# Optimization experiments

Hardware: AMD Instinct MI355X
Metric: run time of the kernel (lower is better)

Reference implementation:

```python
import math
import jax, jax.numpy as jnp
import numpy as np

EMB = 768
N_HEAD = 12
B, T = 8, 1024

def setup_inputs() -> dict:
    key = jax.random.key(0)
    ks = jax.random.split(key, 5)
    x = jax.random.normal(ks[0], (B, T, EMB), dtype=jnp.float32)
    # linear params (torch nn.Linear: y = x @ W.T + b); store as [in, out] for einsum
    s1 = 1.0 / math.sqrt(EMB)
    W_attn = jax.random.uniform(ks[1], (EMB, 3 * EMB), jnp.float32, -s1, s1)
    b_attn = jax.random.uniform(ks[2], (3 * EMB,), jnp.float32, -s1, s1)
    W_proj = jax.random.uniform(ks[3], (EMB, EMB), jnp.float32, -s1, s1)
    b_proj = jax.random.uniform(ks[4], (EMB,), jnp.float32, -s1, s1)
    return {"x": x, "W_attn": W_attn, "b_attn": b_attn, "W_proj": W_proj, "b_proj": b_proj}

def reference(x, W_attn, b_attn, W_proj, b_proj):
    Bb, Tt, C = x.shape
    hd = C // N_HEAD
    qkv = x @ W_attn + b_attn                       # [B,T,3C]
    q, k, v = jnp.split(qkv, 3, axis=-1)
    # [B,T,C] -> [B,H,T,hd]
    def to_heads(t):
        return t.reshape(Bb, Tt, N_HEAD, hd).transpose(0, 2, 1, 3)
    q, k, v = to_heads(q), to_heads(k), to_heads(v)
    scale = 1.0 / math.sqrt(hd)
    scores = jnp.einsum('bhqd,bhkd->bhqk', q, k) * scale   # [B,H,T,T]
    causal = jnp.tril(jnp.ones((Tt, Tt), dtype=bool))
    scores = jnp.where(causal[None, None], scores, jnp.float32(-jnp.inf))
    attn = jax.nn.softmax(scores, axis=-1)
    y = jnp.einsum('bhqk,bhkd->bhqd', attn, v)              # [B,H,T,hd]
    y = y.transpose(0, 2, 1, 3).reshape(Bb, Tt, C)
    return y @ W_proj + b_proj
```

## Files before the change

kernel.cpp:

```cpp
#include <hip/hip_runtime.h>
#include <hip/hip_bf16.h>

typedef __hip_bfloat16 bf16;
typedef __attribute__((ext_vector_type(8))) short  bfrag;
typedef __attribute__((ext_vector_type(4))) float  facc;

#define B_   8
#define T_   1024
#define C_   768
#define H_   12
#define HD_  64
#define M_   (B_ * T_)
#define N3_  (3 * C_)

__device__ __forceinline__ void gload_lds16(const bf16* g, bf16* l) {
    __builtin_amdgcn_global_load_lds((const __attribute__((address_space(1))) void*)g,
                                     (__attribute__((address_space(3))) void*)l, 16, 0, 0);
}

__global__ void cvt_x_kernel(const float* __restrict__ x, bf16* __restrict__ xb) {
    const size_t i = ((size_t)blockIdx.x * 256 + threadIdx.x) * 4;
    const float4 v = *(const float4*)(x + i);
    bf16* o = xb + i;
    o[0] = __float2bfloat16(v.x); o[1] = __float2bfloat16(v.y);
    o[2] = __float2bfloat16(v.z); o[3] = __float2bfloat16(v.w);
}
__global__ void cvt_wT_kernel(const float* __restrict__ w, bf16* __restrict__ wt, int K, int N) {
    __shared__ float tile[32][33];
    const int k0 = blockIdx.y * 32, n0 = blockIdx.x * 32;
    const int tx = threadIdx.x, ty = threadIdx.y;
    for (int i = ty; i < 32; i += 8) tile[i][tx] = w[(size_t)(k0 + i) * N + n0 + tx];
    __syncthreads();
    for (int i = ty; i < 32; i += 8)
        wt[(size_t)(n0 + i) * K + k0 + tx] = __float2bfloat16(tile[tx][i]);
}

#define GEMM_BT_BODY(A, Bt, K_, m0, n0, acc)                                            \
    __shared__ bf16 As[128 * 64];                                                       \
    __shared__ bf16 Bs[128 * 64];                                                       \
    const int t = threadIdx.x, w = t >> 6, lane = t & 63;                               \
    const int wm = (w >> 1) * 64, wn = (w & 1) * 64;                                    \
    const int fr = lane & 15, quad = lane >> 4;                                         \
    const int srow8 = lane >> 3;                                              \
    const int schunk = ((lane & 7) ^ srow8) * 8;               \
    facc acc[4][4];                                                                     \
    for (int i = 0; i < 4; ++i) for (int j = 0; j < 4; ++j)                             \
        for (int r = 0; r < 4; ++r) acc[i][j][r] = 0.f;                                 \
    for (int k0 = 0; k0 < (K_); k0 += 64) {                                             \
        for (int l = 0; l < 4; ++l) {                                                   \
            const int R0 = w * 32 + l * 8;                                              \
            gload_lds16((A)  + (size_t)(m0 + R0 + srow8) * (K_) + k0 + schunk,          \
                        As + R0 * 64 + lane * 8);                                       \
            gload_lds16((Bt) + (size_t)(n0 + R0 + srow8) * (K_) + k0 + schunk,          \
                        Bs + R0 * 64 + lane * 8);                                       \
        }                                                                               \
        __syncthreads();                                                                \
        for (int kk = 0; kk < 2; ++kk) {                                                \
            const int pc = ((kk * 4 + quad) ^ (fr & 7)) * 8;                            \
            bfrag af[4], bfr[4];                                                        \
            for (int i = 0; i < 4; ++i)                                                 \
                af[i] = *(const bfrag*)(As + (wm + i * 16 + fr) * 64 + pc);             \
            for (int j = 0; j < 4; ++j)                                                 \
                bfr[j] = *(const bfrag*)(Bs + (wn + j * 16 + fr) * 64 + pc);            \
            for (int i = 0; i < 4; ++i)                                                 \
                for (int j = 0; j < 4; ++j)                                             \
                    acc[i][j] = __builtin_amdgcn_mfma_f32_16x16x32_bf16(af[i], bfr[j],  \
                                                                        acc[i][j], 0, 0, 0); \
        }                                                                               \
        __syncthreads();                                                                \
    }

__global__ __launch_bounds__(256) void qkv_mfma_kernel(
        const bf16* __restrict__ xb, const bf16* __restrict__ wat,
        const float* __restrict__ bias,
        bf16* __restrict__ Q, bf16* __restrict__ K, bf16* __restrict__ Vt) {
    const int m0 = blockIdx.y * 128, n0 = blockIdx.x * 128;
    GEMM_BT_BODY(xb, wat, C_, m0, n0, acc)
    for (int i = 0; i < 4; ++i) {
        const int row = m0 + wm + i * 16 + quad * 4;
        for (int j = 0; j < 4; ++j) {
            const int col = n0 + wn + j * 16 + fr;
            const float bv = bias[col];
            const int which = col / C_;
            const int cc = col - which * C_;
            const int h = cc >> 6, d = cc & 63;
            for (int r = 0; r < 4; ++r) {
                const int rr = row + r;
                const int bb = rr >> 10, tt = rr & 1023;
                const int bh = bb * H_ + h;
                const bf16 val = __float2bfloat16(acc[i][j][r] + bv);
                if (which == 0)      Q[((size_t)bh * T_ + tt) * HD_ + d] = val;
                else if (which == 1) K[((size_t)bh * T_ + tt) * HD_ + d] = val;
                else                 Vt[((size_t)bh * HD_ + d) * T_ + tt] = val;
            }
        }
    }
}

__global__ __launch_bounds__(256) void proj_mfma_kernel(
        const bf16* __restrict__ y, const bf16* __restrict__ wpt,
        const float* __restrict__ bias, float* __restrict__ out) {
    const int m0 = blockIdx.y * 128, n0 = blockIdx.x * 128;
    GEMM_BT_BODY(y, wpt, C_, m0, n0, acc)
    for (int i = 0; i < 4; ++i) {
        const int row = m0 + wm + i * 16 + quad * 4;
        for (int j = 0; j < 4; ++j) {
            const int col = n0 + wn + j * 16 + fr;
            const float bv = bias[col];
            for (int r = 0; r < 4; ++r)
                out[(size_t)(row + r) * C_ + col] = acc[i][j][r] + bv;
        }
    }
}

__global__ __launch_bounds__(256) void flash_attn_kernel(
        const bf16* __restrict__ Q, const bf16* __restrict__ K,
        const bf16* __restrict__ Vt, bf16* __restrict__ Y) {
    const int id   = blockIdx.x;
    const int bh   = (id & 7) * 12 + ((id >> 3) % 12);
    const int qpair = (id >> 3) / 12;
    const int t = threadIdx.x, w = t >> 6, lane = t & 63;
    const int fr = lane & 15, quad = lane >> 4, fq = quad * 8;

    __shared__ bf16 sK[64 * 64];
    __shared__ bf16 sVt[64 * 64];
    __shared__ bf16 sP[4][16][72];

    const bf16* Kbh = K  + (size_t)bh * T_ * HD_;
    const bf16* Vbh = Vt + (size_t)bh * HD_ * T_;
    const int b_ = bh / H_, h_ = bh % H_;

    const int srow = t >> 3;
    const int sgc  = ((t & 7) ^ (srow & 7)) * 8;
    const int c0   = (quad ^ (fr & 7)) * 8;

    for (int phase = 0; phase < 2; ++phase) {
        const int qt = (phase == 0) ? (15 - qpair) : qpair;
        const int q0 = qt * 64;

        const bf16* qbase = Q + ((size_t)bh * T_ + q0 + w * 16 + fr) * HD_;
        bfrag qa0 = *(const bfrag*)(qbase + fq);
        bfrag qa1 = *(const bfrag*)(qbase + 32 + fq);

        facc o[4];
        for (int nb = 0; nb < 4; ++nb) for (int r = 0; r < 4; ++r) o[nb][r] = 0.f;
        float rowl[4] = {0.f, 0.f, 0.f, 0.f};
        float wm = -1e30f;

        for (int kt = 0; kt <= qt; ++kt) {
            const int k0 = kt * 64;
            gload_lds16(Kbh + (size_t)(k0 + srow) * HD_ + sgc,      sK + t * 8);
            gload_lds16(Kbh + (size_t)(k0 + 32 + srow) * HD_ + sgc, sK + 2048 + t * 8);
            gload_lds16(Vbh + (size_t)srow * T_ + k0 + sgc,         sVt + t * 8);
            gload_lds16(Vbh + (size_t)(srow + 32) * T_ + k0 + sgc,  sVt + 2048 + t * 8);
            __syncthreads();

            facc s[4];
            for (int nb = 0; nb < 4; ++nb) for (int r = 0; r < 4; ++r) s[nb][r] = 0.f;
            for (int nb = 0; nb < 4; ++nb) {
                const bf16* kr = sK + (nb * 16 + fr) * 64;
                bfrag kb0 = *(const bfrag*)(kr + c0);
                bfrag kb1 = *(const bfrag*)(kr + (c0 ^ 32));
                s[nb] = __builtin_amdgcn_mfma_f32_16x16x32_bf16(qa0, kb0, s[nb], 0, 0, 0);
                s[nb] = __builtin_amdgcn_mfma_f32_16x16x32_bf16(qa1, kb1, s[nb], 0, 0, 0);
            }

            const int mrow0 = q0 + w * 16 + quad * 4;
            if (kt == qt) {
                for (int nb = 0; nb < 4; ++nb) {
                    const int n_g = k0 + nb * 16 + fr;
                    for (int r = 0; r < 4; ++r) {
                        const float v = s[nb][r] * 0.125f;
                        s[nb][r] = (n_g > mrow0 + r) ? -1e30f : v;
                    }
                }
            } else {
                for (int nb = 0; nb < 4; ++nb)
                    for (int r = 0; r < 4; ++r) s[nb][r] *= 0.125f;
            }

            float mx = s[0][0];
            for (int nb = 0; nb < 4; ++nb)
                for (int r = 0; r < 4; ++r) mx = fmaxf(mx, s[nb][r]);
            mx = fmaxf(mx, __shfl_xor(mx, 1));
            mx = fmaxf(mx, __shfl_xor(mx, 2));
            mx = fmaxf(mx, __shfl_xor(mx, 4));
            mx = fmaxf(mx, __shfl_xor(mx, 8));
            mx = fmaxf(mx, __shfl_xor(mx, 16));
            mx = fmaxf(mx, __shfl_xor(mx, 32));
            const float newm = fmaxf(wm, mx);
            const float alpha = __expf(wm - newm);
            wm = newm;

            float p[4][4];
            for (int nb = 0; nb < 4; ++nb)
                for (int r = 0; r < 4; ++r) p[nb][r] = __expf(s[nb][r] - newm);
            for (int r = 0; r < 4; ++r)
                rowl[r] = rowl[r] * alpha +
                          (p[0][r] + p[1][r] + p[2][r] + p[3][r]);
            for (int nb = 0; nb < 4; ++nb)
                for (int r = 0; r < 4; ++r) o[nb][r] *= alpha;

            for (int nb = 0; nb < 4; ++nb)
                for (int r = 0; r < 4; ++r)
                    sP[w][quad * 4 + r][nb * 16 + fr] = __float2bfloat16(p[nb][r]);

            {
                bfrag pa0 = *(const bfrag*)(&sP[w][fr][fq]);
                bfrag pa1 = *(const bfrag*)(&sP[w][fr][32 + fq]);
                for (int nb = 0; nb < 4; ++nb) {
                    const bf16* vr = sVt + (nb * 16 + fr) * 64;
                    bfrag vb0 = *(const bfrag*)(vr + c0);
                    bfrag vb1 = *(const bfrag*)(vr + (c0 ^ 32));
                    o[nb] = __builtin_amdgcn_mfma_f32_16x16x32_bf16(pa0, vb0, o[nb], 0, 0, 0);
                    o[nb] = __builtin_amdgcn_mfma_f32_16x16x32_bf16(pa1, vb1, o[nb], 0, 0, 0);
                }
            }
            __syncthreads();
        }

        for (int r = 0; r < 4; ++r) {
            float l = rowl[r];
            l += __shfl_xor(l, 1);
            l += __shfl_xor(l, 2);
            l += __shfl_xor(l, 4);
            l += __shfl_xor(l, 8);
            const float inv = 1.0f / l;
            const int tt = q0 + w * 16 + quad * 4 + r;
            bf16* yrow = Y + ((size_t)b_ * T_ + tt) * C_ + h_ * HD_;
            for (int nb = 0; nb < 4; ++nb)
                yrow[nb * 16 + fr] = __float2bfloat16(o[nb][r] * inv);
        }
    }
}

extern "C" void kernel_launch(void* const* d_in, const int* in_sizes, int n_in,
                              void* d_out, int out_size, void* d_ws, size_t ws_size,
                              hipStream_t stream) {
    const float* x      = (const float*)d_in[0];
    const float* W_attn = (const float*)d_in[1];
    const float* b_attn = (const float*)d_in[2];
    const float* W_proj = (const float*)d_in[3];
    const float* b_proj = (const float*)d_in[4];
    float* out = (float*)d_out;

    const size_t per = (size_t)B_ * H_ * T_ * HD_;
    bf16* Q   = (bf16*)d_ws;
    bf16* K   = Q + per;
    bf16* Vt  = K + per;
    bf16* XbY = Vt + per;
    bf16* WaT = XbY + per;
    bf16* WpT = WaT + (size_t)N3_ * C_;

    cvt_x_kernel<<<dim3((M_ * C_) / (256 * 4)), dim3(256), 0, stream>>>(x, XbY);
    cvt_wT_kernel<<<dim3(N3_ / 32, C_ / 32), dim3(32, 8), 0, stream>>>(W_attn, WaT, C_, N3_);
    cvt_wT_kernel<<<dim3(C_ / 32, C_ / 32), dim3(32, 8), 0, stream>>>(W_proj, WpT, C_, C_);

    qkv_mfma_kernel<<<dim3(N3_ / 128, M_ / 128), dim3(256), 0, stream>>>(
        XbY, WaT, b_attn, Q, K, Vt);
    flash_attn_kernel<<<dim3(768), dim3(256), 0, stream>>>(Q, K, Vt, XbY);
    proj_mfma_kernel<<<dim3(C_ / 128, M_ / 128), dim3(256), 0, stream>>>(
        XbY, WpT, b_proj, out);
}
```

Measured before the change: 213.4 us.

## Share K/V tiles across paired query tiles and merge conversion kernels

The flash attention kernel now handles its high and low query tiles together. Each loaded K/V tile is used by both query tiles, so the low tile no longer reloads the shared prefix of keys. The three conversion kernels are merged into one launch to cut launch overhead. In exchange the kernel holds two sets of accumulators, which raises register pressure and may lower occupancy.

```diff
diff --git a/kernel.cpp b/kernel.cpp
--- a/kernel.cpp
+++ b/kernel.cpp
@@ -18,21 +18,32 @@
                                      (__attribute__((address_space(3))) void*)l, 16, 0, 0);
 }
 
-__global__ void cvt_x_kernel(const float* __restrict__ x, bf16* __restrict__ xb) {
-    const size_t i = ((size_t)blockIdx.x * 256 + threadIdx.x) * 4;
-    const float4 v = *(const float4*)(x + i);
-    bf16* o = xb + i;
-    o[0] = __float2bfloat16(v.x); o[1] = __float2bfloat16(v.y);
-    o[2] = __float2bfloat16(v.z); o[3] = __float2bfloat16(v.w);
-}
-__global__ void cvt_wT_kernel(const float* __restrict__ w, bf16* __restrict__ wt, int K, int N) {
+#define XBLK 6144
+#define WABLK 1728
+__global__ __launch_bounds__(256) void cvt_all_kernel(
+        const float* __restrict__ x,  bf16* __restrict__ xb,
+        const float* __restrict__ wa, bf16* __restrict__ wat,
+        const float* __restrict__ wp, bf16* __restrict__ wpt) {
+    const int bid = blockIdx.x, t = threadIdx.x;
+    if (bid < XBLK) {
+        const size_t i = ((size_t)bid * 256 + t) * 4;
+        const float4 v = *(const float4*)(x + i);
+        bf16* o = xb + i;
+        o[0] = __float2bfloat16(v.x); o[1] = __float2bfloat16(v.y);
+        o[2] = __float2bfloat16(v.z); o[3] = __float2bfloat16(v.w);
+        return;
+    }
     __shared__ float tile[32][33];
-    const int k0 = blockIdx.y * 32, n0 = blockIdx.x * 32;
-    const int tx = threadIdx.x, ty = threadIdx.y;
+    const float* w; bf16* wt; int N, tI;
+    if (bid < XBLK + WABLK) { w = wa; wt = wat; N = N3_; tI = bid - XBLK; }
+    else                    { w = wp; wt = wpt; N = C_;  tI = bid - XBLK - WABLK; }
+    const int ntn = N / 32;
+    const int n0 = (tI % ntn) * 32, k0 = (tI / ntn) * 32;
+    const int tx = t & 31, ty = t >> 5;
     for (int i = ty; i < 32; i += 8) tile[i][tx] = w[(size_t)(k0 + i) * N + n0 + tx];
     __syncthreads();
     for (int i = ty; i < 32; i += 8)
-        wt[(size_t)(n0 + i) * K + k0 + tx] = __float2bfloat16(tile[tx][i]);
+        wt[(size_t)(n0 + i) * C_ + k0 + tx] = __float2bfloat16(tile[tx][i]);
 }
 
 #define GEMM_BT_BODY(A, Bt, K_, m0, n0, acc)                                            \
@@ -116,9 +127,10 @@
 __global__ __launch_bounds__(256) void flash_attn_kernel(
         const bf16* __restrict__ Q, const bf16* __restrict__ K,
         const bf16* __restrict__ Vt, bf16* __restrict__ Y) {
-    const int id   = blockIdx.x;
-    const int bh   = (id & 7) * 12 + ((id >> 3) % 12);
+    const int id    = blockIdx.x;
+    const int bh    = (id & 7) * 12 + ((id >> 3) % 12);
     const int qpair = (id >> 3) / 12;
+    const int qtH = 15 - qpair, qtL = qpair;
     const int t = threadIdx.x, w = t >> 6, lane = t & 63;
     const int fr = lane & 15, quad = lane >> 4, fq = quad * 8;
 
@@ -134,91 +146,92 @@
     const int sgc  = ((t & 7) ^ (srow & 7)) * 8;
     const int c0   = (quad ^ (fr & 7)) * 8;
 
-    for (int phase = 0; phase < 2; ++phase) {
-        const int qt = (phase == 0) ? (15 - qpair) : qpair;
-        const int q0 = qt * 64;
-
-        const bf16* qbase = Q + ((size_t)bh * T_ + q0 + w * 16 + fr) * HD_;
-        bfrag qa0 = *(const bfrag*)(qbase + fq);
-        bfrag qa1 = *(const bfrag*)(qbase + 32 + fq);
-
-        facc o[4];
-        for (int nb = 0; nb < 4; ++nb) for (int r = 0; r < 4; ++r) o[nb][r] = 0.f;
-        float rowl[4] = {0.f, 0.f, 0.f, 0.f};
-        float wm = -1e30f;
-
-        for (int kt = 0; kt <= qt; ++kt) {
-            const int k0 = kt * 64;
-            gload_lds16(Kbh + (size_t)(k0 + srow) * HD_ + sgc,      sK + t * 8);
-            gload_lds16(Kbh + (size_t)(k0 + 32 + srow) * HD_ + sgc, sK + 2048 + t * 8);
-            gload_lds16(Vbh + (size_t)srow * T_ + k0 + sgc,         sVt + t * 8);
-            gload_lds16(Vbh + (size_t)(srow + 32) * T_ + k0 + sgc,  sVt + 2048 + t * 8);
-            __syncthreads();
-
-            facc s[4];
-            for (int nb = 0; nb < 4; ++nb) for (int r = 0; r < 4; ++r) s[nb][r] = 0.f;
+    const bf16* qbH = Q + ((size_t)bh * T_ + qtH * 64 + w * 16 + fr) * HD_;
+    const bf16* qbL = Q + ((size_t)bh * T_ + qtL * 64 + w * 16 + fr) * HD_;
+    bfrag qaH0 = *(const bfrag*)(qbH + fq), qaH1 = *(const bfrag*)(qbH + 32 + fq);
+    bfrag qaL0 = *(const bfrag*)(qbL + fq), qaL1 = *(const bfrag*)(qbL + 32 + fq);
+
+    facc oH[4], oL[4];
+    float rlH[4] = {0.f, 0.f, 0.f, 0.f}, rlL[4] = {0.f, 0.f, 0.f, 0.f};
+    float wmH = -1e30f, wmL = -1e30f;
+    for (int nb = 0; nb < 4; ++nb)
+        for (int r = 0; r < 4; ++r) { oH[nb][r] = 0.f; oL[nb][r] = 0.f; }
+
+    auto tile_step = [&](int kt, int qt, int q0, bfrag qa0, bfrag qa1,
+                         facc (&o)[4], float (&rowl)[4], float& wmax) {
+        const int k0 = kt * 64;
+        facc s[4];
+        for (int nb = 0; nb < 4; ++nb) for (int r = 0; r < 4; ++r) s[nb][r] = 0.f;
+        for (int nb = 0; nb < 4; ++nb) {
+            const bf16* kr = sK + (nb * 16 + fr) * 64;
+            bfrag kb0 = *(const bfrag*)(kr + c0);
+            bfrag kb1 = *(const bfrag*)(kr + (c0 ^ 32));
+            s[nb] = __builtin_amdgcn_mfma_f32_16x16x32_bf16(qa0, kb0, s[nb], 0, 0, 0);
+            s[nb] = __builtin_amdgcn_mfma_f32_16x16x32_bf16(qa1, kb1, s[nb], 0, 0, 0);
+        }
+        const int mrow0 = q0 + w * 16 + quad * 4;
+        if (kt == qt) {
             for (int nb = 0; nb < 4; ++nb) {
-                const bf16* kr = sK + (nb * 16 + fr) * 64;
-                bfrag kb0 = *(const bfrag*)(kr + c0);
-                bfrag kb1 = *(const bfrag*)(kr + (c0 ^ 32));
-                s[nb] = __builtin_amdgcn_mfma_f32_16x16x32_bf16(qa0, kb0, s[nb], 0, 0, 0);
-                s[nb] = __builtin_amdgcn_mfma_f32_16x16x32_bf16(qa1, kb1, s[nb], 0, 0, 0);
-            }
-
-            const int mrow0 = q0 + w * 16 + quad * 4;
-            if (kt == qt) {
-                for (int nb = 0; nb < 4; ++nb) {
-                    const int n_g = k0 + nb * 16 + fr;
-                    for (int r = 0; r < 4; ++r) {
-                        const float v = s[nb][r] * 0.125f;
-                        s[nb][r] = (n_g > mrow0 + r) ? -1e30f : v;
-                    }
-                }
-            } else {
-                for (int nb = 0; nb < 4; ++nb)
-                    for (int r = 0; r < 4; ++r) s[nb][r] *= 0.125f;
-            }
-
-            float mx = s[0][0];
-            for (int nb = 0; nb < 4; ++nb)
-                for (int r = 0; r < 4; ++r) mx = fmaxf(mx, s[nb][r]);
-            mx = fmaxf(mx, __shfl_xor(mx, 1));
-            mx = fmaxf(mx, __shfl_xor(mx, 2));
-            mx = fmaxf(mx, __shfl_xor(mx, 4));
-            mx = fmaxf(mx, __shfl_xor(mx, 8));
-            mx = fmaxf(mx, __shfl_xor(mx, 16));
-            mx = fmaxf(mx, __shfl_xor(mx, 32));
-            const float newm = fmaxf(wm, mx);
-            const float alpha = __expf(wm - newm);
-            wm = newm;
-
-            float p[4][4];
-            for (int nb = 0; nb < 4; ++nb)
-                for (int r = 0; r < 4; ++r) p[nb][r] = __expf(s[nb][r] - newm);
-            for (int r = 0; r < 4; ++r)
-                rowl[r] = rowl[r] * alpha +
-                          (p[0][r] + p[1][r] + p[2][r] + p[3][r]);
-            for (int nb = 0; nb < 4; ++nb)
-                for (int r = 0; r < 4; ++r) o[nb][r] *= alpha;
-
-            for (int nb = 0; nb < 4; ++nb)
-                for (int r = 0; r < 4; ++r)
-                    sP[w][quad * 4 + r][nb * 16 + fr] = __float2bfloat16(p[nb][r]);
-
-            {
-                bfrag pa0 = *(const bfrag*)(&sP[w][fr][fq]);
-                bfrag pa1 = *(const bfrag*)(&sP[w][fr][32 + fq]);
-                for (int nb = 0; nb < 4; ++nb) {
-                    const bf16* vr = sVt + (nb * 16 + fr) * 64;
-                    bfrag vb0 = *(const bfrag*)(vr + c0);
-                    bfrag vb1 = *(const bfrag*)(vr + (c0 ^ 32));
-                    o[nb] = __builtin_amdgcn_mfma_f32_16x16x32_bf16(pa0, vb0, o[nb], 0, 0, 0);
-                    o[nb] = __builtin_amdgcn_mfma_f32_16x16x32_bf16(pa1, vb1, o[nb], 0, 0, 0);
+                const int n_g = k0 + nb * 16 + fr;
+                for (int r = 0; r < 4; ++r) {
+                    const float v = s[nb][r] * 0.125f;
+                    s[nb][r] = (n_g > mrow0 + r) ? -1e30f : v;
                 }
             }
-            __syncthreads();
-        }
-
+        } else {
+            for (int nb = 0; nb < 4; ++nb)
+                for (int r = 0; r < 4; ++r) s[nb][r] *= 0.125f;
+        }
+        float mx = s[0][0];
+        for (int nb = 0; nb < 4; ++nb)
+            for (int r = 0; r < 4; ++r) mx = fmaxf(mx, s[nb][r]);
+        mx = fmaxf(mx, __shfl_xor(mx, 1));
+        mx = fmaxf(mx, __shfl_xor(mx, 2));
+        mx = fmaxf(mx, __shfl_xor(mx, 4));
+        mx = fmaxf(mx, __shfl_xor(mx, 8));
+        mx = fmaxf(mx, __shfl_xor(mx, 16));
+        mx = fmaxf(mx, __shfl_xor(mx, 32));
+        const float newm = fmaxf(wmax, mx);
+        const float alpha = __expf(wmax - newm);
+        wmax = newm;
+        float p[4][4];
+        for (int nb = 0; nb < 4; ++nb)
+            for (int r = 0; r < 4; ++r) p[nb][r] = __expf(s[nb][r] - newm);
+        for (int r = 0; r < 4; ++r)
+            rowl[r] = rowl[r] * alpha + (p[0][r] + p[1][r] + p[2][r] + p[3][r]);
+        for (int nb = 0; nb < 4; ++nb)
+            for (int r = 0; r < 4; ++r) o[nb][r] *= alpha;
+        for (int nb = 0; nb < 4; ++nb)
+            for (int r = 0; r < 4; ++r)
+                sP[w][quad * 4 + r][nb * 16 + fr] = __float2bfloat16(p[nb][r]);
+        bfrag pa0 = *(const bfrag*)(&sP[w][fr][fq]);
+        bfrag pa1 = *(const bfrag*)(&sP[w][fr][32 + fq]);
+        for (int nb = 0; nb < 4; ++nb) {
+            const bf16* vr = sVt + (nb * 16 + fr) * 64;
+            bfrag vb0 = *(const bfrag*)(vr + c0);
+            bfrag vb1 = *(const bfrag*)(vr + (c0 ^ 32));
+            o[nb] = __builtin_amdgcn_mfma_f32_16x16x32_bf16(pa0, vb0, o[nb], 0, 0, 0);
+            o[nb] = __builtin_amdgcn_mfma_f32_16x16x32_bf16(pa1, vb1, o[nb], 0, 0, 0);
+        }
+    };
+
+    for (int kt = 0; kt <= qtH; ++kt) {
+        const int k0 = kt * 64;
+        gload_lds16(Kbh + (size_t)(k0 + srow) * HD_ + sgc,      sK + t * 8);
+        gload_lds16(Kbh + (size_t)(k0 + 32 + srow) * HD_ + sgc, sK + 2048 + t * 8);
+        gload_lds16(Vbh + (size_t)srow * T_ + k0 + sgc,         sVt + t * 8);
+        gload_lds16(Vbh + (size_t)(srow + 32) * T_ + k0 + sgc,  sVt + 2048 + t * 8);
+        __syncthreads();
+        tile_step(kt, qtH, qtH * 64, qaH0, qaH1, oH, rlH, wmH);
+        if (kt <= qtL)
+            tile_step(kt, qtL, qtL * 64, qaL0, qaL1, oL, rlL, wmL);
+        __syncthreads();
+    }
+
+    for (int which = 0; which < 2; ++which) {
+        const int q0 = (which == 0) ? qtH * 64 : qtL * 64;
+        facc* o = (which == 0) ? oH : oL;
+        float* rowl = (which == 0) ? rlH : rlL;
         for (int r = 0; r < 4; ++r) {
             float l = rowl[r];
             l += __shfl_xor(l, 1);
@@ -252,10 +265,8 @@
     bf16* WaT = XbY + per;
     bf16* WpT = WaT + (size_t)N3_ * C_;
 
-    cvt_x_kernel<<<dim3((M_ * C_) / (256 * 4)), dim3(256), 0, stream>>>(x, XbY);
-    cvt_wT_kernel<<<dim3(N3_ / 32, C_ / 32), dim3(32, 8), 0, stream>>>(W_attn, WaT, C_, N3_);
-    cvt_wT_kernel<<<dim3(C_ / 32, C_ / 32), dim3(32, 8), 0, stream>>>(W_proj, WpT, C_, C_);
-
+    cvt_all_kernel<<<dim3(XBLK + WABLK + 576), dim3(256), 0, stream>>>(
+        x, XbY, W_attn, WaT, W_proj, WpT);
     qkv_mfma_kernel<<<dim3(N3_ / 128, M_ / 128), dim3(256), 0, stream>>>(
         XbY, WaT, b_attn, Q, K, Vt);
     flash_attn_kernel<<<dim3(768), dim3(256), 0, stream>>>(Q, K, Vt, XbY);
```

Measured after the change: 223.5 us. 1.05x slower.
